# Performance work log

Hardware: AMD Instinct MI355X
Metric: run time of the kernel (lower is better)

Reference implementation:

```python
import jax, jax.numpy as jnp
import numpy as np

B, T, C = 2, 2048, 2048
H = 16          # n_head == n_kv_head
HD = 128        # head_size = hidden_dim // n_head (nope/value dim)
RD = 64         # qk_rope_head_dim
QLR = 1536      # q_lora_rank
KLR = 512       # kv_lora_rank
BASE = 10000.0
SCALE = (HD + RD) ** -0.5  # mscale = 1.0 since rope_scale = 1.0
EPS = 1e-6


def _rms(x, w):
    return x * jax.lax.rsqrt(jnp.mean(x * x, axis=-1, keepdims=True) + EPS) * w


def _rope_cos_sin(seq_len, dim):
    inv_freq = 1.0 / (BASE ** (jnp.arange(0, dim, 2, dtype=jnp.float32) / dim))
    t = jnp.arange(seq_len, dtype=jnp.float32)
    freqs = jnp.outer(t, inv_freq)            # [T, dim/2]
    emb = jnp.concatenate([freqs, freqs], -1)  # [T, dim]
    return jnp.cos(emb), jnp.sin(emb)


def _rotate_half(x):
    h = x.shape[-1] // 2
    return jnp.concatenate([-x[..., h:], x[..., :h]], axis=-1)


def setup_inputs() -> dict:
    key = jax.random.key(0)
    ks = jax.random.split(key, 8)
    s = 0.02
    return {
        "x": jax.random.normal(ks[0], (B, T, C), jnp.float32),
        "Wq_down": jax.random.normal(ks[1], (C, QLR), jnp.float32) * s,
        "q_norm_w": jnp.ones((QLR,), jnp.float32),
        "Wq_up": jax.random.normal(ks[2], (QLR, H * HD), jnp.float32) * s,
        "Wq_pe": jax.random.normal(ks[3], (QLR, H * RD), jnp.float32) * s,
        "Wkv_down": jax.random.normal(ks[4], (C, KLR), jnp.float32) * s,
        "kv_norm_w": jnp.ones((KLR,), jnp.float32),
        "Wkv_up": jax.random.normal(ks[5], (KLR, H * 2 * HD), jnp.float32) * s,
        "Wk_pe": jax.random.normal(ks[6], (C, RD), jnp.float32) * s,
        "k_pe_norm_w": jnp.ones((RD,), jnp.float32),
        "Wo": jax.random.normal(ks[7], (H * HD, C), jnp.float32) * s,
    }


def reference(x, Wq_down, q_norm_w, Wq_up, Wq_pe, Wkv_down, kv_norm_w,
              Wkv_up, Wk_pe, k_pe_norm_w, Wo):
    # ---- low-rank Q path ----
    cQ = _rms(x @ Wq_down, q_norm_w)                      # [B,T,QLR]
    q_nop = (cQ @ Wq_up).reshape(B, T, H, HD).transpose(0, 2, 1, 3)   # [B,H,T,HD]
    q_pe = (cQ @ Wq_pe).reshape(B, T, H, RD).transpose(0, 2, 1, 3)    # [B,H,T,RD]
    # ---- low-rank KV path ----
    cKV = _rms(x @ Wkv_down, kv_norm_w)                   # [B,T,KLR]
    kv = cKV @ Wkv_up                                     # [B,T,H*2*HD]
    k_nop, v = jnp.split(kv, 2, axis=-1)
    k_nop = k_nop.reshape(B, T, H, HD).transpose(0, 2, 1, 3)          # [B,H,T,HD]
    v = v.reshape(B, T, H, HD).transpose(0, 2, 1, 3)                  # [B,H,T,HD]
    # ---- decoupled RoPE key (shared across heads) ----
    k_pe = _rms(x @ Wk_pe, k_pe_norm_w).reshape(B, T, 1, RD).transpose(0, 2, 1, 3)  # [B,1,T,RD]
    cos, sin = _rope_cos_sin(T, RD)                       # [T,RD]
    q_pe = q_pe * cos + _rotate_half(q_pe) * sin
    k_pe = k_pe * cos + _rotate_half(k_pe) * sin
    # ---- concat nope + rope, causal SDPA ----
    q = jnp.concatenate([q_nop, q_pe], axis=-1)                           # [B,H,T,HD+RD]
    k = jnp.concatenate([k_nop, jnp.broadcast_to(k_pe, (B, H, T, RD))], axis=-1)
    scores = jnp.einsum('bhqd,bhkd->bhqk', q, k) * SCALE
    mask = jnp.tril(jnp.ones((T, T), dtype=bool))
    scores = jnp.where(mask, scores, jnp.finfo(scores.dtype).min)
    attn = jax.nn.softmax(scores, axis=-1)
    y = jnp.einsum('bhqk,bhkd->bhqd', attn, v)                            # [B,H,T,HD]
    y = y.transpose(0, 2, 1, 3).reshape(B, T, H * HD)
    return y @ Wo
```

## Files before the change

kernel.cpp:

```cpp
#include <hip/hip_runtime.h>
#include <hip/hip_bf16.h>
#include <cmath>

typedef __hip_bfloat16 bf16;
typedef __attribute__((ext_vector_type(8))) short s16x8;
typedef __attribute__((ext_vector_type(4))) float f32x4;

#define B_   2
#define T_   2048
#define C_   2048
#define H_   16
#define HD_  128
#define RD_  64
#define QLR_ 1536
#define KLR_ 512
#define SCALE_ 0.07216878364870322f

static __device__ __forceinline__ float b2f(bf16 v){ return __bfloat162float(v); }
static __device__ __forceinline__ bf16  f2b(float v){ return __float2bfloat16(v); }
static __device__ __forceinline__ float us2f(unsigned short u){
    union { unsigned short s[2]; float f; } v; v.s[0]=0; v.s[1]=u; return v.f;
}
static __device__ __forceinline__ float ldS(const void* p, size_t i, int isf32){
    return isf32 ? ((const float*)p)[i] : b2f(((const bf16*)p)[i]);
}
static __device__ __forceinline__ void ld4(const void* p, size_t i, int isf32, float* o){
    if (isf32) {
        float4 v = *(const float4*)((const float*)p + i);
        o[0]=v.x; o[1]=v.y; o[2]=v.z; o[3]=v.w;
    } else {
        ushort4 u = *(const ushort4*)((const bf16*)p + i);
        o[0]=us2f(u.x); o[1]=us2f(u.y); o[2]=us2f(u.z); o[3]=us2f(u.w);
    }
}

__global__ __launch_bounds__(64) void detect_kernel(const unsigned short* __restrict__ x,
                                                    int* __restrict__ flag)
{
    int big = 0;
    for (int i = threadIdx.x; i < 1024; i += 64) {
        const unsigned short u = x[2*i];
        const int e = (u >> 7) & 0xFF;
        if (e >= 139) big++;
    }
    #pragma unroll
    for (int off = 32; off; off >>= 1) big += __shfl_down(big, off, 64);
    if (threadIdx.x == 0) *flag = (big > 8) ? 1 : 0;
}

__global__ __launch_bounds__(256) void convert_kernel(const void* __restrict__ in,
                                                      bf16* __restrict__ out, int n,
                                                      const int* __restrict__ flag)
{
    const int f = *flag;
    const int i0 = (blockIdx.x * 256 + threadIdx.x) * 8;
    if (i0 >= n) return;
    float v[8];
    ld4(in, i0, f, v);
    ld4(in, i0 + 4, f, v + 4);
    bf16* o = out + i0;
    #pragma unroll
    for (int k = 0; k < 8; ++k) o[k] = f2b(v[k]);
}

struct TDesc { const void* in; bf16* out; int R, Cc, blkStart, nx; };
struct TBatch { TDesc d[5]; int nseg; };

__global__ __launch_bounds__(256) void transpose_batch(TBatch tb,
                                                       const int* __restrict__ flag)
{
    const int f = *flag;
    const int bid = blockIdx.x;
    int s = 0;
    #pragma unroll
    for (int i = 1; i < 5; ++i)
        if (i < tb.nseg && bid >= tb.d[i].blkStart) s = i;
    const TDesc d = tb.d[s];
    const int local = bid - d.blkStart;
    const int c0 = (local % d.nx) * 32;
    const int r0 = (local / d.nx) * 32;

    __shared__ float tile[32][33];
    const int tx = threadIdx.x & 31, ty = threadIdx.x >> 5;
    #pragma unroll
    for (int i = 0; i < 4; ++i)
        tile[ty + 8*i][tx] = ldS(d.in, (size_t)(r0 + ty + 8*i) * d.Cc + c0 + tx, f);
    __syncthreads();
    #pragma unroll
    for (int i = 0; i < 4; ++i)
        d.out[(size_t)(c0 + ty + 8*i) * d.R + r0 + tx] = f2b(tile[tx][ty + 8*i]);
}

__global__ __launch_bounds__(256) void transpose_v_kernel(const bf16* __restrict__ kvb,
                                                          bf16* __restrict__ vT)
{
    __shared__ bf16 tile[32][34];
    const int c0 = blockIdx.x * 32;
    const int r0 = blockIdx.y * 32;
    const int tx = threadIdx.x & 31, ty = threadIdx.x >> 5;
    #pragma unroll
    for (int i = 0; i < 4; ++i)
        tile[ty + 8*i][tx] = kvb[(size_t)(r0 + ty + 8*i) * (H_*256) + H_*128 + c0 + tx];
    __syncthreads();
    const int b  = r0 >> 11;
    const int t0 = r0 & (T_ - 1);
    #pragma unroll
    for (int i = 0; i < 4; ++i) {
        const int c  = c0 + ty + 8*i;
        const int hh = c >> 7, dd = c & 127;
        vT[(((size_t)b*H_ + hh)*HD_ + dd)*T_ + t0 + tx] = tile[tx][ty + 8*i];
    }
}

struct GOuts { void* p[3]; int start[3]; int stride[3]; int nseg; };

__global__ __launch_bounds__(256) void mfma_gemm(const bf16* __restrict__ A,
                                                 const bf16* __restrict__ BT,
                                                 GOuts go, int N, int K,
                                                 const int* __restrict__ flag, int cH)
{
    const int cf = cH ? *flag : 0;
    __shared__ bf16 As[128 * 32];
    __shared__ bf16 Bs[128 * 32];
    const int tid  = threadIdx.x;
    const int w    = tid >> 6;
    const int lane = tid & 63;
    const int quad = lane >> 4;
    const int l16  = lane & 15;
    const int wm   = w >> 1, wn = w & 1;
    const int bm   = blockIdx.y * 128, bn = blockIdx.x * 128;
    const int lrow = lane >> 2;
    const int lk   = (lane & 3) * 8;

    int seg = 0;
    #pragma unroll
    for (int i = 1; i < 3; ++i)
        if (i < go.nseg && bn >= go.start[i]) seg = i;
    void* const dstp   = go.p[seg];
    const int  dstoff  = go.start[seg];
    const int  dstride = go.stride[seg];

    f32x4 acc[4][4];
    #pragma unroll
    for (int i = 0; i < 4; ++i)
        #pragma unroll
        for (int j = 0; j < 4; ++j)
            acc[i][j] = (f32x4){0.f, 0.f, 0.f, 0.f};

    for (int kk = 0; kk < K; kk += 32) {
        if (kk) __syncthreads();
        #pragma unroll
        for (int c = 0; c < 2; ++c) {
            const int ch  = w * 2 + c;
            const int row = ch * 16 + lrow;
            const bf16* g = A + (size_t)(bm + row) * K + kk + lk;
            __builtin_amdgcn_global_load_lds(
                (const __attribute__((address_space(1))) unsigned int*)g,
                (__attribute__((address_space(3))) unsigned int*)(As + ch * 512),
                16, 0, 0);
        }
        #pragma unroll
        for (int c = 0; c < 2; ++c) {
            const int ch  = w * 2 + c;
            const int row = ch * 16 + lrow;
            const bf16* g = BT + (size_t)(bn + row) * K + kk + lk;
            __builtin_amdgcn_global_load_lds(
                (const __attribute__((address_space(1))) unsigned int*)g,
                (__attribute__((address_space(3))) unsigned int*)(Bs + ch * 512),
                16, 0, 0);
        }
        __syncthreads();

        s16x8 af[4], bfv[4];
        #pragma unroll
        for (int i = 0; i < 4; ++i)
            af[i] = *(const s16x8*)&As[(wm*64 + i*16 + l16) * 32 + quad*8];
        #pragma unroll
        for (int j = 0; j < 4; ++j)
            bfv[j] = *(const s16x8*)&Bs[(wn*64 + j*16 + l16) * 32 + quad*8];
        #pragma unroll
        for (int i = 0; i < 4; ++i)
            #pragma unroll
            for (int j = 0; j < 4; ++j)
                acc[i][j] = __builtin_amdgcn_mfma_f32_16x16x32_bf16(af[i], bfv[j], acc[i][j], 0, 0, 0);
    }

    #pragma unroll
    for (int i = 0; i < 4; ++i) {
        const int crow = bm + wm*64 + i*16 + quad*4;
        #pragma unroll
        for (int r = 0; r < 4; ++r) {
            #pragma unroll
            for (int j = 0; j < 4; ++j) {
                const int ccol = bn + wn*64 + j*16 + l16;
                if (ccol < N) {
                    const size_t idx = (size_t)(crow + r) * dstride + (ccol - dstoff);
                    if (cf) ((float*)dstp)[idx] = acc[i][j][r];
                    else    ((bf16*)dstp)[idx] = f2b(acc[i][j][r]);
                }
            }
        }
    }
}

template<int NPER>
__global__ __launch_bounds__(256) void rms_kernel(bf16* __restrict__ X,
                                                  const void* __restrict__ w,
                                                  const int* __restrict__ flag)
{
    const int wf = *flag;
    const int ncols = NPER * 256;
    __shared__ float red[4];
    const int row = blockIdx.x;
    const int tid = threadIdx.x;
    bf16* xr = X + (size_t)row * ncols;
    float vals[NPER];
    float ss = 0.f;
    #pragma unroll
    for (int i = 0; i < NPER; ++i) {
        float v = b2f(xr[tid + i*256]);
        vals[i] = v; ss += v*v;
    }
    #pragma unroll
    for (int off = 32; off; off >>= 1) ss += __shfl_down(ss, off, 64);
    if ((tid & 63) == 0) red[tid >> 6] = ss;
    __syncthreads();
    const float tot = red[0]+red[1]+red[2]+red[3];
    const float rs  = rsqrtf(tot / (float)ncols + 1e-6f);
    #pragma unroll
    for (int i = 0; i < NPER; ++i) {
        const int c = tid + i*256;
        xr[c] = f2b(vals[i] * rs * ldS(w, c, wf));
    }
}

__global__ __launch_bounds__(64) void kpe_rms_rope(bf16* __restrict__ X,
                                                   const void* __restrict__ w,
                                                   const int* __restrict__ flag)
{
    const int wf   = *flag;
    const int row  = blockIdx.x;
    const int t    = row & (T_ - 1);
    const int lane = threadIdx.x;
    bf16* xr = X + (size_t)row * RD_;
    const float v = b2f(xr[lane]);
    float ss = v * v;
    #pragma unroll
    for (int off = 32; off; off >>= 1) ss += __shfl_down(ss, off, 64);
    ss = __shfl(ss, 0, 64);
    const float rs = rsqrtf(ss / 64.f + 1e-6f);
    const float xn = v * rs * ldS(w, lane, wf);
    const int   i  = lane & 31;
    const float freq = powf(10000.f, -(float)(2*i) / 64.f);
    const float ang  = (float)t * freq;
    const float s = sinf(ang), c = cosf(ang);
    const float other = __shfl_xor(xn, 32, 64);
    const float o = (lane < 32) ? (xn * c - other * s) : (other * s + xn * c);
    xr[lane] = f2b(o);
}

__global__ __launch_bounds__(256) void qpe_rope(bf16* __restrict__ X)
{
    const int row = blockIdx.x;
    const int t   = row & (T_ - 1);
    bf16* xr = X + (size_t)row * (H_ * RD_);
    const int tid = threadIdx.x;
    #pragma unroll
    for (int pp = 0; pp < 2; ++pp) {
        const int p  = tid + pp * 256;
        const int hh = p >> 5;
        const int i  = p & 31;
        const int i0 = hh * 64 + i;
        const int i1 = i0 + 32;
        const float x1 = b2f(xr[i0]), x2 = b2f(xr[i1]);
        const float freq = powf(10000.f, -(float)(2*i) / 64.f);
        const float ang  = (float)t * freq;
        const float s = sinf(ang), c = cosf(ang);
        xr[i0] = f2b(x1 * c - x2 * s);
        xr[i1] = f2b(x1 * s + x2 * c);
    }
}

__global__ __launch_bounds__(256, 2) void flash_attn(const bf16* __restrict__ qnop,
                                                     const bf16* __restrict__ qpe,
                                                     const bf16* __restrict__ kv,
                                                     const bf16* __restrict__ kpe,
                                                     const bf16* __restrict__ vT,
                                                     bf16* __restrict__ y)
{
    __shared__ __align__(16) short Klds[64][200];
    __shared__ __align__(16) short Vt[128][72];
    __shared__ __align__(16) short Plds[4][16][72];

    const int h   = blockIdx.x;
    const int qt  = 31 - (int)blockIdx.y;
    const int b   = blockIdx.z;
    const int q0  = qt * 64;
    const int tid = threadIdx.x;
    const int w    = tid >> 6;
    const int lane = tid & 63;
    const int quad = lane >> 4;
    const int l16  = lane & 15;
    const int row0 = q0 + w * 16;
    const size_t bT = (size_t)b * T_;
    const int bh  = b * H_ + h;

    const int kR = tid >> 4, kC = (tid & 15) * 8;
    const int pR = tid >> 3, pC = (tid & 7) * 8;
    const int vD = tid >> 3, vC = (tid & 7) * 8;

    const bf16* gK = kv  + (bT + kR) * (H_*256) + h*128 + kC;
    const bf16* gP = kpe + (bT + pR) * RD_ + pC;
    const bf16* gV = vT  + ((size_t)bh*HD_ + vD) * T_ + vC;

    s16x8 aq[6];
    {
        const size_t r = bT + row0 + l16;
        const bf16* qn = qnop + r * (H_*128) + h*128 + quad*8;
        #pragma unroll
        for (int kk = 0; kk < 4; ++kk) aq[kk] = *(const s16x8*)(qn + kk*32);
        const bf16* qp = qpe + r * (H_*64) + h*64 + quad*8;
        aq[4] = *(const s16x8*)(qp);
        aq[5] = *(const s16x8*)(qp + 32);
    }

    f32x4 o[8];
    #pragma unroll
    for (int i = 0; i < 8; ++i) o[i] = (f32x4){0.f,0.f,0.f,0.f};
    float m_run[4] = {-1e30f,-1e30f,-1e30f,-1e30f};
    float l_run[4] = {0.f,0.f,0.f,0.f};

    uint4 k0, k1, k2, k3, p0, p1, v0, v1, v2, v3;
    #define PF(J0) do {                                                     \
        const bf16* a_ = gK + (size_t)(J0) * (H_*256);                      \
        k0 = *(const uint4*)(a_);                                           \
        k1 = *(const uint4*)(a_ + 16*(H_*256));                             \
        k2 = *(const uint4*)(a_ + 32*(H_*256));                             \
        k3 = *(const uint4*)(a_ + 48*(H_*256));                             \
        const bf16* p_ = gP + (size_t)(J0) * RD_;                           \
        p0 = *(const uint4*)(p_);                                           \
        p1 = *(const uint4*)(p_ + 32*RD_);                                  \
        const bf16* v_ = gV + (J0);                                         \
        v0 = *(const uint4*)(v_);                                           \
        v1 = *(const uint4*)(v_ + 32*T_);                                   \
        v2 = *(const uint4*)(v_ + 64*T_);                                   \
        v3 = *(const uint4*)(v_ + 96*T_);                                   \
    } while (0)

    PF(0);

    const int ntiles = qt + 1;
    for (int it = 0; it < ntiles; ++it) {
        const int j0 = it * 64;
        asm volatile("s_waitcnt lgkmcnt(0)\n\ts_barrier" ::: "memory");

        *(uint4*)&Klds[kR     ][kC]      = k0;
        *(uint4*)&Klds[kR + 16][kC]      = k1;
        *(uint4*)&Klds[kR + 32][kC]      = k2;
        *(uint4*)&Klds[kR + 48][kC]      = k3;
        *(uint4*)&Klds[pR     ][128+pC]  = p0;
        *(uint4*)&Klds[pR + 32][128+pC]  = p1;
        *(uint4*)&Vt[vD     ][vC]        = v0;
        *(uint4*)&Vt[vD + 32][vC]        = v1;
        *(uint4*)&Vt[vD + 64][vC]        = v2;
        *(uint4*)&Vt[vD + 96][vC]        = v3;

        if (it + 1 < ntiles) PF(j0 + 64);

        asm volatile("s_waitcnt lgkmcnt(0)\n\ts_barrier" ::: "memory");

        if (j0 <= row0 + 15) {
            const bool needmask = (j0 + 63 > row0);
            f32x4 s[4];
            #pragma unroll
            for (int nsub = 0; nsub < 4; ++nsub) {
                f32x4 acc = (f32x4){0.f,0.f,0.f,0.f};
                #pragma unroll
                for (int kk = 0; kk < 6; ++kk) {
                    const s16x8 bk = *(const s16x8*)&Klds[nsub*16 + l16][kk*32 + quad*8];
                    acc = __builtin_amdgcn_mfma_f32_16x16x32_bf16(aq[kk], bk, acc, 0, 0, 0);
                }
                #pragma unroll
                for (int reg = 0; reg < 4; ++reg) acc[reg] *= SCALE_;
                s[nsub] = acc;
            }
            if (needmask) {
                #pragma unroll
                for (int nsub = 0; nsub < 4; ++nsub)
                    #pragma unroll
                    for (int reg = 0; reg < 4; ++reg) {
                        const int col = j0 + nsub*16 + l16;
                        const int row = row0 + quad*4 + reg;
                        if (col > row) s[nsub][reg] = -1e30f;
                    }
            }
            float mt[4], alpha[4], rs[4];
            #pragma unroll
            for (int reg = 0; reg < 4; ++reg)
                mt[reg] = fmaxf(fmaxf(s[0][reg], s[1][reg]), fmaxf(s[2][reg], s[3][reg]));
            #pragma unroll
            for (int d = 1; d < 16; d <<= 1)
                #pragma unroll
                for (int reg = 0; reg < 4; ++reg)
                    mt[reg] = fmaxf(mt[reg], __shfl_xor(mt[reg], d, 64));
            #pragma unroll
            for (int reg = 0; reg < 4; ++reg) {
                const float mnew = fmaxf(m_run[reg], mt[reg]);
                alpha[reg] = __expf(m_run[reg] - mnew);
                m_run[reg] = mnew;
                rs[reg] = 0.f;
            }
            #pragma unroll
            for (int nsub = 0; nsub < 4; ++nsub)
                #pragma unroll
                for (int reg = 0; reg < 4; ++reg) {
                    const float p = __expf(s[nsub][reg] - m_run[reg]);
                    s[nsub][reg] = p;
                    rs[reg] += p;
                }
            #pragma unroll
            for (int d = 1; d < 16; d <<= 1)
                #pragma unroll
                for (int reg = 0; reg < 4; ++reg)
                    rs[reg] += __shfl_xor(rs[reg], d, 64);
            #pragma unroll
            for (int reg = 0; reg < 4; ++reg)
                l_run[reg] = l_run[reg] * alpha[reg] + rs[reg];

            #pragma unroll
            for (int nsub = 0; nsub < 4; ++nsub)
                #pragma unroll
                for (int reg = 0; reg < 4; ++reg) {
                    const bf16 pv = f2b(s[nsub][reg]);
                    Plds[w][quad*4 + reg][nsub*16 + l16] = *(const short*)&pv;
                }
            #pragma unroll
            for (int n2 = 0; n2 < 8; ++n2)
                #pragma unroll
                for (int reg = 0; reg < 4; ++reg)
                    o[n2][reg] *= alpha[reg];

            const s16x8 ap0 = *(const s16x8*)&Plds[w][l16][quad*8];
            const s16x8 ap1 = *(const s16x8*)&Plds[w][l16][32 + quad*8];
            #pragma unroll
            for (int n2 = 0; n2 < 8; ++n2) {
                const s16x8 bv0 = *(const s16x8*)&Vt[n2*16 + l16][quad*8];
                const s16x8 bv1 = *(const s16x8*)&Vt[n2*16 + l16][32 + quad*8];
                o[n2] = __builtin_amdgcn_mfma_f32_16x16x32_bf16(ap0, bv0, o[n2], 0, 0, 0);
                o[n2] = __builtin_amdgcn_mfma_f32_16x16x32_bf16(ap1, bv1, o[n2], 0, 0, 0);
            }
        }
    }
    #undef PF

    #pragma unroll
    for (int reg = 0; reg < 4; ++reg) {
        const float inv = 1.f / l_run[reg];
        const size_t r = bT + row0 + quad*4 + reg;
        bf16* yr = y + r * (H_*128) + h*128 + l16;
        #pragma unroll
        for (int n2 = 0; n2 < 8; ++n2)
            yr[n2*16] = f2b(o[n2][reg] * inv);
    }
}

extern "C" void kernel_launch(void* const* d_in, const int* in_sizes, int n_in,
                              void* d_out, int out_size, void* d_ws, size_t ws_size,
                              hipStream_t stream)
{
    const void* x         = d_in[0];
    const void* Wq_down   = d_in[1];
    const void* q_norm_w  = d_in[2];
    const void* Wq_up     = d_in[3];
    const void* Wq_pe     = d_in[4];
    const void* Wkv_down  = d_in[5];
    const void* kv_norm_w = d_in[6];
    const void* Wkv_up    = d_in[7];
    const void* Wk_pe     = d_in[8];
    const void* kpe_nw    = d_in[9];
    const void* Wo        = d_in[10];

    char* ws = (char*)d_ws;
    int*  flag = (int*)(ws + 0);
    bf16* xb   = (bf16*)(ws + 256);
    bf16* cQ   = (bf16*)(ws + 16777472);
    bf16* cKV  = (bf16*)(ws + 29360384);
    bf16* kpeb = (bf16*)(ws + 33554688);
    bf16* qnop = (bf16*)(ws + 34078976);
    bf16* qpeb = (bf16*)(ws + 50856192);
    bf16* kvb  = (bf16*)(ws + 59244800);
    bf16* yb   = (bf16*)(ws + 92799232);

    bf16* P1 = kvb;
    bf16* P2 = (bf16*)((char*)kvb + 8912896);
    bf16* P3 = cQ;
    bf16* P4 = (bf16*)((char*)cQ + 4194304);
    bf16* vT = xb;

    const dim3 blk(256);

    detect_kernel<<<1, dim3(64), 0, stream>>>((const unsigned short*)x, flag);
    convert_kernel<<<(B_*T_*C_)/(256*8), blk, 0, stream>>>(x, xb, B_*T_*C_, flag);

    {
        TBatch tb;
        tb.d[0] = { Wq_down,  P1,               C_,  QLR_,     0, QLR_/32 };
        tb.d[1] = { Wkv_down, P1 + 1536*2048,   C_,  KLR_,  3072, KLR_/32 };
        tb.d[2] = { Wk_pe,    P1 + 2048*2048,   C_,  RD_,   4096, RD_/32  };
        tb.d[3] = { Wq_up,    P2,               QLR_, 2048, 4224, 2048/32 };
        tb.d[4] = { Wq_pe,    P2 + 2048*1536,   QLR_, 1024, 7296, 1024/32 };
        tb.nseg = 5;
        transpose_batch<<<8832, blk, 0, stream>>>(tb, flag);
    }

    {
        GOuts go; go.nseg = 3;
        go.p[0]=cQ;   go.start[0]=0;    go.stride[0]=QLR_;
        go.p[1]=cKV;  go.start[1]=1536; go.stride[1]=KLR_;
        go.p[2]=kpeb; go.start[2]=2048; go.stride[2]=RD_;
        mfma_gemm<<<dim3(17, 32), blk, 0, stream>>>(xb, P1, go, 2112, C_, flag, 0);
    }
    rms_kernel<6><<<B_*T_, blk, 0, stream>>>(cQ, q_norm_w, flag);
    rms_kernel<2><<<B_*T_, blk, 0, stream>>>(cKV, kv_norm_w, flag);
    kpe_rms_rope<<<B_*T_, dim3(64), 0, stream>>>(kpeb, kpe_nw, flag);

    {
        GOuts go; go.nseg = 2;
        go.p[0]=qnop; go.start[0]=0;    go.stride[0]=H_*HD_;
        go.p[1]=qpeb; go.start[1]=2048; go.stride[1]=H_*RD_;
        go.p[2]=nullptr; go.start[2]=0; go.stride[2]=0;
        mfma_gemm<<<dim3(24, 32), blk, 0, stream>>>(cQ, P2, go, 3072, QLR_, flag, 0);
    }
    qpe_rope<<<B_*T_, blk, 0, stream>>>(qpeb);

    {
        TBatch tb;
        tb.d[0] = { Wkv_up, P3, KLR_, H_*2*HD_,    0, (H_*2*HD_)/32 };
        tb.d[1] = { Wo,     P4, H_*HD_, C_,     2048, C_/32 };
        tb.d[2] = tb.d[1]; tb.d[3] = tb.d[1]; tb.d[4] = tb.d[1];
        tb.nseg = 2;
        transpose_batch<<<6144, blk, 0, stream>>>(tb, flag);
    }

    {
        GOuts go; go.nseg = 1;
        go.p[0]=kvb; go.start[0]=0; go.stride[0]=H_*2*HD_;
        go.p[1]=nullptr; go.start[1]=0; go.stride[1]=0;
        go.p[2]=nullptr; go.start[2]=0; go.stride[2]=0;
        mfma_gemm<<<dim3(32, 32), blk, 0, stream>>>(cKV, P3, go, H_*2*HD_, KLR_, flag, 0);
    }
    transpose_v_kernel<<<dim3((H_*HD_)/32, (B_*T_)/32), blk, 0, stream>>>(kvb, vT);

    flash_attn<<<dim3(H_, T_/64, B_), blk, 0, stream>>>(qnop, qpeb, kvb, kpeb, vT, yb);

    {
        GOuts go; go.nseg = 1;
        go.p[0]=d_out; go.start[0]=0; go.stride[0]=C_;
        go.p[1]=nullptr; go.start[1]=0; go.stride[1]=0;
        go.p[2]=nullptr; go.start[2]=0; go.stride[2]=0;
        mfma_gemm<<<dim3(C_/128, 32), blk, 0, stream>>>(yb, P4, go, C_, H_*HD_, flag, 1);
    }
}
```

Measured before the change: 509.6 us.

## Swizzle flash-attention LDS tiles, fold scale into exp2, skip unneeded rescales

Replaces the padded shared-memory K, V and P tiles with unpadded tiles whose 16-byte chunks are XOR-swizzled. This avoids bank conflicts while cutting LDS use, and the launch bound rises from 2 to 3 blocks per SM to use the freed space. The softmax folds the attention scale and log2(e) into a single fma feeding exp2. When no row max in the wavefront grows, it skips the alpha exponentials and the rescaling of the output accumulators. The larger occupancy target may force register spilling, and the wave-wide branch adds a little divergence logic.

```diff
diff --git a/kernel.cpp b/kernel.cpp
--- a/kernel.cpp
+++ b/kernel.cpp
@@ -15,6 +15,7 @@
 #define QLR_ 1536
 #define KLR_ 512
 #define SCALE_ 0.07216878364870322f
+#define C1_ (SCALE_ * 1.4426950408889634f)
 
 static __device__ __forceinline__ float b2f(bf16 v){ return __bfloat162float(v); }
 static __device__ __forceinline__ bf16  f2b(float v){ return __float2bfloat16(v); }
@@ -281,16 +282,16 @@
     }
 }
 
-__global__ __launch_bounds__(256, 2) void flash_attn(const bf16* __restrict__ qnop,
+__global__ __launch_bounds__(256, 3) void flash_attn(const bf16* __restrict__ qnop,
                                                      const bf16* __restrict__ qpe,
                                                      const bf16* __restrict__ kv,
                                                      const bf16* __restrict__ kpe,
                                                      const bf16* __restrict__ vT,
                                                      bf16* __restrict__ y)
 {
-    __shared__ __align__(16) short Klds[64][200];
-    __shared__ __align__(16) short Vt[128][72];
-    __shared__ __align__(16) short Plds[4][16][72];
+    __shared__ __align__(16) short Klds[64 * 192];
+    __shared__ __align__(16) short Vt[128 * 64];
+    __shared__ __align__(16) short Plds[4][16 * 64];
 
     const int h   = blockIdx.x;
     const int qt  = 31 - (int)blockIdx.y;
@@ -301,17 +302,23 @@
     const int lane = tid & 63;
     const int quad = lane >> 4;
     const int l16  = lane & 15;
+    const int rk   = l16 & 7;
+    const int rkp  = (l16 ^ (l16 >> 3)) & 7;
     const int row0 = q0 + w * 16;
     const size_t bT = (size_t)b * T_;
     const int bh  = b * H_ + h;
 
-    const int kR = tid >> 4, kC = (tid & 15) * 8;
-    const int pR = tid >> 3, pC = (tid & 7) * 8;
-    const int vD = tid >> 3, vC = (tid & 7) * 8;
-
-    const bf16* gK = kv  + (bT + kR) * (H_*256) + h*128 + kC;
-    const bf16* gP = kpe + (bT + pR) * RD_ + pC;
-    const bf16* gV = vT  + ((size_t)bh*HD_ + vD) * T_ + vC;
+    const int kR = tid >> 4, kS = tid & 15;
+    const int pR = tid >> 3, pS = tid & 7;
+    const int vD = tid >> 3, vS = tid & 7;
+
+    const bf16* gK = kv  + (bT + kR) * (H_*256) + h*128 + kS*8;
+    const bf16* gP = kpe + (bT + pR) * RD_ + pS*8;
+    const bf16* gV = vT  + ((size_t)bh*HD_ + vD) * T_ + vS*8;
+
+    short* const wK = &Klds[kR*192 + ((kS ^ (kR & 7)) << 3)];
+    short* const wP = &Klds[pR*192 + 128 + ((pS ^ (pR & 7)) << 3)];
+    short* const wV = &Vt[vD*64 + ((vS ^ (vD & 7)) << 3)];
 
     s16x8 aq[6];
     {
@@ -354,16 +361,16 @@
         const int j0 = it * 64;
         asm volatile("s_waitcnt lgkmcnt(0)\n\ts_barrier" ::: "memory");
 
-        *(uint4*)&Klds[kR     ][kC]      = k0;
-        *(uint4*)&Klds[kR + 16][kC]      = k1;
-        *(uint4*)&Klds[kR + 32][kC]      = k2;
-        *(uint4*)&Klds[kR + 48][kC]      = k3;
-        *(uint4*)&Klds[pR     ][128+pC]  = p0;
-        *(uint4*)&Klds[pR + 32][128+pC]  = p1;
-        *(uint4*)&Vt[vD     ][vC]        = v0;
-        *(uint4*)&Vt[vD + 32][vC]        = v1;
-        *(uint4*)&Vt[vD + 64][vC]        = v2;
-        *(uint4*)&Vt[vD + 96][vC]        = v3;
+        *(uint4*)(wK)          = k0;
+        *(uint4*)(wK + 16*192) = k1;
+        *(uint4*)(wK + 32*192) = k2;
+        *(uint4*)(wK + 48*192) = k3;
+        *(uint4*)(wP)          = p0;
+        *(uint4*)(wP + 32*192) = p1;
+        *(uint4*)(wV)          = v0;
+        *(uint4*)(wV + 32*64)  = v1;
+        *(uint4*)(wV + 64*64)  = v2;
+        *(uint4*)(wV + 96*64)  = v3;
 
         if (it + 1 < ntiles) PF(j0 + 64);
 
@@ -377,11 +384,10 @@
                 f32x4 acc = (f32x4){0.f,0.f,0.f,0.f};
                 #pragma unroll
                 for (int kk = 0; kk < 6; ++kk) {
-                    const s16x8 bk = *(const s16x8*)&Klds[nsub*16 + l16][kk*32 + quad*8];
+                    const s16x8 bk = *(const s16x8*)&Klds[(nsub*16 + l16)*192
+                                        + ((((kk << 2) | quad) ^ rk) << 3)];
                     acc = __builtin_amdgcn_mfma_f32_16x16x32_bf16(aq[kk], bk, acc, 0, 0, 0);
                 }
-                #pragma unroll
-                for (int reg = 0; reg < 4; ++reg) acc[reg] *= SCALE_;
                 s[nsub] = acc;
             }
             if (needmask) {
@@ -403,18 +409,31 @@
                 #pragma unroll
                 for (int reg = 0; reg < 4; ++reg)
                     mt[reg] = fmaxf(mt[reg], __shfl_xor(mt[reg], d, 64));
+
+            bool growl = false;
             #pragma unroll
             for (int reg = 0; reg < 4; ++reg) {
                 const float mnew = fmaxf(m_run[reg], mt[reg]);
-                alpha[reg] = __expf(m_run[reg] - mnew);
-                m_run[reg] = mnew;
-                rs[reg] = 0.f;
-            }
+                growl |= (mnew > m_run[reg]);
+                alpha[reg] = mnew;
+            }
+            const bool grow = __any((int)growl);
+            if (grow) {
+                #pragma unroll
+                for (int reg = 0; reg < 4; ++reg) {
+                    const float a = __builtin_amdgcn_exp2f((m_run[reg] - alpha[reg]) * C1_);
+                    m_run[reg] = alpha[reg];
+                    alpha[reg] = a;
+                }
+            }
+            float nm[4];
+            #pragma unroll
+            for (int reg = 0; reg < 4; ++reg) { nm[reg] = -m_run[reg] * C1_; rs[reg] = 0.f; }
             #pragma unroll
             for (int nsub = 0; nsub < 4; ++nsub)
                 #pragma unroll
                 for (int reg = 0; reg < 4; ++reg) {
-                    const float p = __expf(s[nsub][reg] - m_run[reg]);
+                    const float p = __builtin_amdgcn_exp2f(__builtin_fmaf(s[nsub][reg], C1_, nm[reg]));
                     s[nsub][reg] = p;
                     rs[reg] += p;
                 }
@@ -423,29 +442,40 @@
                 #pragma unroll
                 for (int reg = 0; reg < 4; ++reg)
                     rs[reg] += __shfl_xor(rs[reg], d, 64);
-            #pragma unroll
-            for (int reg = 0; reg < 4; ++reg)
-                l_run[reg] = l_run[reg] * alpha[reg] + rs[reg];
+            if (grow) {
+                #pragma unroll
+                for (int reg = 0; reg < 4; ++reg)
+                    l_run[reg] = l_run[reg] * alpha[reg] + rs[reg];
+            } else {
+                #pragma unroll
+                for (int reg = 0; reg < 4; ++reg)
+                    l_run[reg] += rs[reg];
+            }
 
             #pragma unroll
             for (int nsub = 0; nsub < 4; ++nsub)
                 #pragma unroll
                 for (int reg = 0; reg < 4; ++reg) {
                     const bf16 pv = f2b(s[nsub][reg]);
-                    Plds[w][quad*4 + reg][nsub*16 + l16] = *(const short*)&pv;
+                    const int prow = (quad << 2) + reg;
+                    const int pk   = (prow ^ (prow >> 3)) & 7;
+                    const int pby  = ((nsub << 5) + (l16 << 1)) ^ (pk << 4);
+                    Plds[w][prow*64 + (pby >> 1)] = *(const short*)&pv;
                 }
-            #pragma unroll
-            for (int n2 = 0; n2 < 8; ++n2)
-                #pragma unroll
-                for (int reg = 0; reg < 4; ++reg)
-                    o[n2][reg] *= alpha[reg];
-
-            const s16x8 ap0 = *(const s16x8*)&Plds[w][l16][quad*8];
-            const s16x8 ap1 = *(const s16x8*)&Plds[w][l16][32 + quad*8];
+            if (grow) {
+                #pragma unroll
+                for (int n2 = 0; n2 < 8; ++n2)
+                    #pragma unroll
+                    for (int reg = 0; reg < 4; ++reg)
+                        o[n2][reg] *= alpha[reg];
+            }
+
+            const s16x8 ap0 = *(const s16x8*)&Plds[w][l16*64 + (((quad    ) ^ rkp) << 3)];
+            const s16x8 ap1 = *(const s16x8*)&Plds[w][l16*64 + (((quad | 4) ^ rkp) << 3)];
             #pragma unroll
             for (int n2 = 0; n2 < 8; ++n2) {
-                const s16x8 bv0 = *(const s16x8*)&Vt[n2*16 + l16][quad*8];
-                const s16x8 bv1 = *(const s16x8*)&Vt[n2*16 + l16][32 + quad*8];
+                const s16x8 bv0 = *(const s16x8*)&Vt[(n2*16 + l16)*64 + (((quad    ) ^ rk) << 3)];
+                const s16x8 bv1 = *(const s16x8*)&Vt[(n2*16 + l16)*64 + (((quad | 4) ^ rk) << 3)];
                 o[n2] = __builtin_amdgcn_mfma_f32_16x16x32_bf16(ap0, bv0, o[n2], 0, 0, 0);
                 o[n2] = __builtin_amdgcn_mfma_f32_16x16x32_bf16(ap1, bv1, o[n2], 0, 0, 0);
             }
```

Result: slower. 543.9 us (+6.7%).
